# Performance work log

Measured on AMD Instinct MI355X. Metric: run time of the kernel, lower is better.

The kernel has to match this reference:

```python
import jax, jax.numpy as jnp
import numpy as np

B, S, D = 16, 1024, 384
H, DH = 6, 64  # head_dim = hidden // heads


def setup_inputs() -> dict:
    key = jax.random.key(0)
    ks = jax.random.split(key, 9)
    std = 0.02
    return {
        "x": jax.random.normal(ks[0], (B, S, D), jnp.float32),
        "Wq": jax.random.normal(ks[1], (H, D, DH), jnp.float32) * std,
        "bq": jax.random.normal(ks[2], (H, DH), jnp.float32) * std,
        "Wk": jax.random.normal(ks[3], (H, D, DH), jnp.float32) * std,
        "bk": jax.random.normal(ks[4], (H, DH), jnp.float32) * std,
        "Wv": jax.random.normal(ks[5], (H, D, DH), jnp.float32) * std,
        "bv": jax.random.normal(ks[6], (H, DH), jnp.float32) * std,
        "Wo": jax.random.normal(ks[7], (D, D), jnp.float32) * std,  # [out, in] like nn.Linear
        "bo": jax.random.normal(ks[8], (D,), jnp.float32) * std,
    }


def reference(x, Wq, bq, Wk, bk, Wv, bv, Wo, bo):
    # Per-head q/k/v projections (stacked over heads h)
    q = jnp.einsum("bsd,hde->bhse", x, Wq) + bq[None, :, None, :]
    k = jnp.einsum("bsd,hde->bhse", x, Wk) + bk[None, :, None, :]
    v = jnp.einsum("bsd,hde->bhse", x, Wv) + bv[None, :, None, :]
    # Explicit softmax attention (dropout prob = 0.0 in config)
    scores = jnp.einsum("bhse,bhte->bhst", q, k) / jnp.sqrt(jnp.float32(DH))
    probs = jax.nn.softmax(scores, axis=-1)
    ctx = jnp.einsum("bhst,bhte->bhse", probs, v)  # [B,H,S,DH]
    # Concat heads along last dim: [B,S,H*DH]
    concat = jnp.transpose(ctx, (0, 2, 1, 3)).reshape(B, S, H * DH)
    # Output projection (nn.Linear: y = x @ W^T + b)
    out = jnp.einsum("bsd,ed->bse", concat, Wo) + bo
    return out
```

## Files before the change

kernel.cpp:

```cpp
#include <hip/hip_runtime.h>
#include <hip/hip_bf16.h>

typedef __attribute__((ext_vector_type(8))) short short8;
typedef __attribute__((ext_vector_type(4))) short short4v;
typedef __attribute__((ext_vector_type(4))) float float4v;

#define MFMA16(a,b,c) __builtin_amdgcn_mfma_f32_16x16x32_bf16((a),(b),(c),0,0,0)
#define EXP2(x) __builtin_amdgcn_exp2f(x)

static constexpr int Bz = 16, Sq = 1024, Dm = 384, Hh = 6, Dh = 64;
static constexpr int Mtok = Bz * Sq;
static constexpr int NQKV = 1152;

__device__ __forceinline__ short f2bf(float f) {
  union { float f; unsigned u; } v; v.f = f;
  unsigned r = v.u + 0x7fffu + ((v.u >> 16) & 1u);
  return (short)(r >> 16);
}

__device__ __forceinline__ void gload16(const void* src, void* lds) {
  __builtin_amdgcn_global_load_lds(
      (const __attribute__((address_space(1))) unsigned int*)src,
      (__attribute__((address_space(3))) unsigned int*)lds, 16, 0, 0);
}

__global__ __launch_bounds__(256) void conv_x(const float* __restrict__ x,
                                              short* __restrict__ xb) {
  const int i = (blockIdx.x * 256 + threadIdx.x) * 8;
  float4v v0 = *(const float4v*)(x + i);
  float4v v1 = *(const float4v*)(x + i + 4);
  short8 o;
  o[0] = f2bf(v0[0]); o[1] = f2bf(v0[1]); o[2] = f2bf(v0[2]); o[3] = f2bf(v0[3]);
  o[4] = f2bf(v1[0]); o[5] = f2bf(v1[1]); o[6] = f2bf(v1[2]); o[7] = f2bf(v1[3]);
  *(short8*)(xb + i) = o;
}

__global__ __launch_bounds__(256) void conv_w(const float* __restrict__ Wq,
                                              const float* __restrict__ Wk,
                                              const float* __restrict__ Wv,
                                              const float* __restrict__ bq,
                                              const float* __restrict__ bk,
                                              const float* __restrict__ bv,
                                              const float* __restrict__ Wo,
                                              short* __restrict__ Wt,
                                              float* __restrict__ bias,
                                              short* __restrict__ Wob) {
  const float SCL = 0.125f * 1.44269504088896340736f;
  const int i = blockIdx.x * 256 + threadIdx.x;
  const int NW = NQKV * Dm;
  if (i < NW) {
    const int c = i / Dm, d = i % Dm;
    const int p = c / 384, rr = c % 384;
    const int h = rr >> 6, dh = rr & 63;
    const float* W = (p == 0) ? Wq : ((p == 1) ? Wk : Wv);
    float w = W[(h * Dm + d) * Dh + dh];
    if (p == 0) w *= SCL;
    Wt[c * Dm + d] = f2bf(w);
  } else if (i < NW + NQKV) {
    const int c = i - NW;
    const int p = c / 384, rr = c % 384;
    const int h = rr >> 6, dh = rr & 63;
    const float* bb = (p == 0) ? bq : ((p == 1) ? bk : bv);
    float b = bb[h * Dh + dh];
    if (p == 0) b *= SCL;
    bias[c] = b;
  } else if (i < NW + NQKV + Dm * Dm) {
    const int j = i - NW - NQKV;
    Wob[j] = f2bf(Wo[j]);
  }
}


__global__ __launch_bounds__(256) void qkv_gemm(const short* __restrict__ Xb,
                                                const short* __restrict__ Wt,
                                                const float* __restrict__ bias,
                                                short* __restrict__ qkv,
                                                short* __restrict__ vt) {
  __shared__ char smem[32768];
  const int tid = threadIdx.x;
  const int wave = tid >> 6, lane = tid & 63;
  const int r = lane & 15, g = lane >> 4;
  const int wr = wave >> 1, wc = wave & 1;

  const int flat = blockIdx.x;
  const int w = (flat & 7) * 144 + (flat >> 3);
  const int bx = w % 9, by = w / 9;
  const int bm0 = by * 128, bn0 = bx * 128;
  const int m0 = bm0 + wr * 64, n0 = bn0 + wc * 64;

  float bv_n[4];
#pragma unroll
  for (int ni = 0; ni < 4; ++ni) bv_n[ni] = bias[n0 + ni * 16 + r];
  asm volatile("s_waitcnt vmcnt(0)" ::: "memory");

  const char *aSrc0, *aSrc1, *bSrc0, *bSrc1;
  {
    const int o0 = tid * 16, o1 = 4096 + tid * 16;
    const int lr0 = o0 >> 7, cb0 = (o0 & 127) ^ ((lr0 & 7) << 4);
    const int lr1 = o1 >> 7, cb1 = (o1 & 127) ^ ((lr1 & 7) << 4);
    const int m_0 = 2 * lr0 + (cb0 >> 6), kb0 = cb0 & 63;
    const int m_1 = 2 * lr1 + (cb1 >> 6), kb1 = cb1 & 63;
    aSrc0 = (const char*)(Xb + (bm0 + m_0) * Dm) + kb0;
    aSrc1 = (const char*)(Xb + (bm0 + m_1) * Dm) + kb1;
    bSrc0 = (const char*)(Wt + (bn0 + m_0) * Dm) + kb0;
    bSrc1 = (const char*)(Wt + (bn0 + m_1) * Dm) + kb1;
  }
  auto stage = [&](int t, int buf) {
    char* base = smem + buf * 16384;
    const int kb = t * 64;
    gload16(aSrc0 + kb, base + wave * 1024);
    gload16(aSrc1 + kb, base + 4096 + wave * 1024);
    gload16(bSrc0 + kb, base + 8192 + wave * 1024);
    gload16(bSrc1 + kb, base + 12288 + wave * 1024);
  };

  int aOff[4], bOff[4];
#pragma unroll
  for (int i = 0; i < 4; ++i) {
    const int m = wr * 64 + i * 16 + r;
    const int lr = m >> 1;
    aOff[i] = lr * 128 + ((((m & 1) << 6) | (16 * g)) ^ ((lr & 7) << 4));
    const int n = wc * 64 + i * 16 + r;
    const int lrn = n >> 1;
    bOff[i] = 8192 + lrn * 128 + ((((n & 1) << 6) | (16 * g)) ^ ((lrn & 7) << 4));
  }

  float4v acc[4][4] = {};
  auto compute = [&](int buf) {
    const char* sb = smem + buf * 16384;
    short8 a[4], b[4];
#pragma unroll
    for (int i = 0; i < 4; ++i) a[i] = *(const short8*)(sb + aOff[i]);
#pragma unroll
    for (int i = 0; i < 4; ++i) b[i] = *(const short8*)(sb + bOff[i]);
#pragma unroll
    for (int mi = 0; mi < 4; ++mi)
#pragma unroll
      for (int ni = 0; ni < 4; ++ni)
        acc[mi][ni] = MFMA16(a[mi], b[ni], acc[mi][ni]);
  };

  stage(0, 0);
  stage(1, 1);
  for (int t = 0; t < 11; ++t) {
    asm volatile("s_waitcnt vmcnt(4)" ::: "memory");
    __builtin_amdgcn_s_barrier();
    compute(t & 1);
    __builtin_amdgcn_s_barrier();
    if (t < 10) stage(t + 2, t & 1);
  }
  asm volatile("s_waitcnt vmcnt(0)" ::: "memory");
  __builtin_amdgcn_s_barrier();
  compute(1);

#pragma unroll
  for (int ni = 0; ni < 4; ++ni) {
    const int col = n0 + ni * 16 + r;
    const int p = col / 384, rr2 = col % 384;
    const int h = rr2 >> 6, dh = rr2 & 63;
    const float bv = bv_n[ni];
#pragma unroll
    for (int mi = 0; mi < 4; ++mi) {
#pragma unroll
      for (int reg = 0; reg < 4; ++reg) {
        const int mg = m0 + mi * 16 + 4 * g + reg;
        const short o = f2bf(acc[mi][ni][reg] + bv);
        if (p < 2) {
          qkv[mg * NQKV + col] = o;
        } else {
          const int bb = mg >> 10, s = mg & 1023;
          vt[((bb * Hh + h) * Dh + dh) * Sq + s] = o;
        }
      }
    }
  }
}

__global__ __launch_bounds__(256) void attn(const short* __restrict__ qkv,
                                            const short* __restrict__ vt,
                                            short* __restrict__ ctx) {
  __shared__ char smem[32768];
  const int tid = threadIdx.x;
  const int wave = tid >> 6, lane = tid & 63;
  const int r = lane & 15, g = lane >> 4;
  const int xr = (r & 7) << 4;
  const int flat = blockIdx.x;
  const int w = (flat & 7) * 96 + (flat >> 3);
  const int qb = w & 7, bh = w >> 3;
  const int b = bh / Hh, h = bh % Hh;
  const int tok0 = b * Sq;
  const int qw = qb * 128 + wave * 32;

  short8 qf[2][2];
#pragma unroll
  for (int f = 0; f < 2; ++f) {
    const short* qp = qkv + (tok0 + qw + 16 * f + r) * NQKV + h * Dh;
    qf[f][0] = *(const short8*)(qp + 8 * g);
    qf[f][1] = *(const short8*)(qp + 32 + 8 * g);
  }
  asm volatile("s_waitcnt vmcnt(0)" ::: "memory");

  const short* kg = qkv + tok0 * NQKV + 384 + h * Dh;
  const short* vg = vt + (b * Hh + h) * Dh * Sq;

  const int o0 = wave * 2048 + lane * 16;
  const int row0 = o0 >> 7, cb0 = (o0 & 127) ^ ((row0 & 7) << 4);
  const int o1 = o0 + 1024;
  const int row1 = o1 >> 7, cb1 = (o1 & 127) ^ ((row1 & 7) << 4);

#define STAGE(T, BUFSEL)                                                        \
  {                                                                             \
    char* kb_ = smem + (BUFSEL) * 16384;                                        \
    const int kv_ = (T) * 64;                                                   \
    gload16((const char*)(kg + (kv_ + row0) * NQKV) + cb0, kb_ + wave * 2048);  \
    gload16((const char*)(vg + row0 * Sq + kv_) + cb0, kb_ + 8192 + wave * 2048);\
    gload16((const char*)(kg + (kv_ + row1) * NQKV) + cb1, kb_ + wave * 2048 + 1024);\
    gload16((const char*)(vg + row1 * Sq + kv_) + cb1, kb_ + 8192 + wave * 2048 + 1024);\
  }

  int kOff[4][2], vOff[4][2];
#pragma unroll
  for (int kt = 0; kt < 4; ++kt)
#pragma unroll
    for (int c = 0; c < 2; ++c)
      kOff[kt][c] = (16 * kt + r) * 128 + ((64 * c + 16 * g) ^ xr);
#pragma unroll
  for (int d = 0; d < 4; ++d)
#pragma unroll
    for (int h2 = 0; h2 < 2; ++h2)
      vOff[d][h2] = (16 * d + r) * 128 + ((64 * h2 + 8 * g) ^ xr);

  float4v acc[4][2] = {};
  float lsum[2] = {0.f, 0.f};

  auto compute = [&](int bufsel) {
    const char* kb = smem + bufsel * 16384;
    const char* vb = kb + 8192;
    short8 kf[4][2];
#pragma unroll
    for (int kt = 0; kt < 4; ++kt) {
      kf[kt][0] = *(const short8*)(kb + kOff[kt][0]);
      kf[kt][1] = *(const short8*)(kb + kOff[kt][1]);
    }
    short8 vf[4][2];
#pragma unroll
    for (int d = 0; d < 4; ++d)
#pragma unroll
      for (int h2 = 0; h2 < 2; ++h2) {
        short4v lo = *(const short4v*)(vb + vOff[d][h2]);
        short4v hi = *(const short4v*)(vb + (vOff[d][h2] ^ 32));
        short8 t;
        t[0] = lo[0]; t[1] = lo[1]; t[2] = lo[2]; t[3] = lo[3];
        t[4] = hi[0]; t[5] = hi[1]; t[6] = hi[2]; t[7] = hi[3];
        vf[d][h2] = t;
      }
    float4v s[4][2];
#pragma unroll
    for (int kt = 0; kt < 4; ++kt)
#pragma unroll
      for (int f = 0; f < 2; ++f) {
        float4v z = {};
        z = MFMA16(kf[kt][0], qf[f][0], z);
        z = MFMA16(kf[kt][1], qf[f][1], z);
        s[kt][f] = z;
      }
    short8 pa[2][2];
#pragma unroll
    for (int f = 0; f < 2; ++f) {
      float ps = 0.f;
#pragma unroll
      for (int h2 = 0; h2 < 2; ++h2) {
#pragma unroll
        for (int j = 0; j < 4; ++j) {
          const float e0 = EXP2(s[2 * h2][f][j]);
          const float e1 = EXP2(s[2 * h2 + 1][f][j]);
          pa[f][h2][j]     = f2bf(e0);
          pa[f][h2][4 + j] = f2bf(e1);
          ps += e0 + e1;
        }
      }
      lsum[f] += ps;
    }
#pragma unroll
    for (int d = 0; d < 4; ++d)
#pragma unroll
      for (int f = 0; f < 2; ++f) {
        acc[d][f] = MFMA16(pa[f][0], vf[d][0], acc[d][f]);
        acc[d][f] = MFMA16(pa[f][1], vf[d][1], acc[d][f]);
      }
  };

  STAGE(0, 0)
  STAGE(1, 1)
  for (int t = 0; t < 15; ++t) {
    asm volatile("s_waitcnt vmcnt(4)" ::: "memory");
    __builtin_amdgcn_s_barrier();
    compute(t & 1);
    __builtin_amdgcn_s_barrier();
    if (t < 14) STAGE(t + 2, t & 1)
  }
  asm volatile("s_waitcnt vmcnt(0)" ::: "memory");
  __builtin_amdgcn_s_barrier();
  compute(1);

#pragma unroll
  for (int f = 0; f < 2; ++f) {
    lsum[f] += __shfl_xor(lsum[f], 16);
    lsum[f] += __shfl_xor(lsum[f], 32);
  }
#pragma unroll
  for (int f = 0; f < 2; ++f) {
    float il[4];
#pragma unroll
    for (int reg = 0; reg < 4; ++reg) il[reg] = 1.f / __shfl(lsum[f], 4 * g + reg);
#pragma unroll
    for (int d = 0; d < 4; ++d) {
      short* cp = ctx + (tok0 + qw + 16 * f + 4 * g) * Dm + h * Dh + 16 * d + r;
#pragma unroll
      for (int reg = 0; reg < 4; ++reg)
        cp[reg * Dm] = f2bf(acc[d][f][reg] * il[reg]);
    }
  }
}

__global__ __launch_bounds__(256) void out_gemm(const short* __restrict__ ctx,
                                                const short* __restrict__ Wob,
                                                const float* __restrict__ bo,
                                                float* __restrict__ out) {
  __shared__ char smem[32768];
  const int tid = threadIdx.x;
  const int wave = tid >> 6, lane = tid & 63;
  const int r = lane & 15, g = lane >> 4;
  const int wr = wave >> 1, wc = wave & 1;

  const int flat = blockIdx.x;
  const int w = (flat & 7) * 48 + (flat >> 3);
  const int bx = w % 3, by = w / 3;
  const int bm0 = by * 128, bn0 = bx * 128;
  const int m0 = bm0 + wr * 64, n0 = bn0 + wc * 64;

  float bv_n[4];
#pragma unroll
  for (int ni = 0; ni < 4; ++ni) bv_n[ni] = bo[n0 + ni * 16 + r];
  asm volatile("s_waitcnt vmcnt(0)" ::: "memory");

  const char *aSrc0, *aSrc1, *bSrc0, *bSrc1;
  {
    const int o0 = tid * 16, o1 = 4096 + tid * 16;
    const int lr0 = o0 >> 7, cb0 = (o0 & 127) ^ ((lr0 & 7) << 4);
    const int lr1 = o1 >> 7, cb1 = (o1 & 127) ^ ((lr1 & 7) << 4);
    const int m_0 = 2 * lr0 + (cb0 >> 6), kb0 = cb0 & 63;
    const int m_1 = 2 * lr1 + (cb1 >> 6), kb1 = cb1 & 63;
    aSrc0 = (const char*)(ctx + (bm0 + m_0) * Dm) + kb0;
    aSrc1 = (const char*)(ctx + (bm0 + m_1) * Dm) + kb1;
    bSrc0 = (const char*)(Wob + (bn0 + m_0) * Dm) + kb0;
    bSrc1 = (const char*)(Wob + (bn0 + m_1) * Dm) + kb1;
  }
  auto stage = [&](int t, int buf) {
    char* base = smem + buf * 16384;
    const int kb = t * 64;
    gload16(aSrc0 + kb, base + wave * 1024);
    gload16(aSrc1 + kb, base + 4096 + wave * 1024);
    gload16(bSrc0 + kb, base + 8192 + wave * 1024);
    gload16(bSrc1 + kb, base + 12288 + wave * 1024);
  };

  int aOff[4], bOff[4];
#pragma unroll
  for (int i = 0; i < 4; ++i) {
    const int m = wr * 64 + i * 16 + r;
    const int lr = m >> 1;
    aOff[i] = lr * 128 + ((((m & 1) << 6) | (16 * g)) ^ ((lr & 7) << 4));
    const int n = wc * 64 + i * 16 + r;
    const int lrn = n >> 1;
    bOff[i] = 8192 + lrn * 128 + ((((n & 1) << 6) | (16 * g)) ^ ((lrn & 7) << 4));
  }

  float4v acc[4][4] = {};
  auto compute = [&](int buf) {
    const char* sb = smem + buf * 16384;
    short8 a[4], b[4];
#pragma unroll
    for (int i = 0; i < 4; ++i) a[i] = *(const short8*)(sb + aOff[i]);
#pragma unroll
    for (int i = 0; i < 4; ++i) b[i] = *(const short8*)(sb + bOff[i]);
#pragma unroll
    for (int mi = 0; mi < 4; ++mi)
#pragma unroll
      for (int ni = 0; ni < 4; ++ni)
        acc[mi][ni] = MFMA16(a[mi], b[ni], acc[mi][ni]);
  };

  stage(0, 0);
  stage(1, 1);
  for (int t = 0; t < 11; ++t) {
    asm volatile("s_waitcnt vmcnt(4)" ::: "memory");
    __builtin_amdgcn_s_barrier();
    compute(t & 1);
    __builtin_amdgcn_s_barrier();
    if (t < 10) stage(t + 2, t & 1);
  }
  asm volatile("s_waitcnt vmcnt(0)" ::: "memory");
  __builtin_amdgcn_s_barrier();
  compute(1);

#pragma unroll
  for (int ni = 0; ni < 4; ++ni) {
    const int col = n0 + ni * 16 + r;
    const float bv = bv_n[ni];
#pragma unroll
    for (int mi = 0; mi < 4; ++mi) {
#pragma unroll
      for (int reg = 0; reg < 4; ++reg) {
        const int mg = m0 + mi * 16 + 4 * g + reg;
        out[mg * Dm + col] = acc[mi][ni][reg] + bv;
      }
    }
  }
}

extern "C" void kernel_launch(void* const* d_in, const int* in_sizes, int n_in,
                              void* d_out, int out_size, void* d_ws, size_t ws_size,
                              hipStream_t stream) {
  const float* x  = (const float*)d_in[0];
  const float* Wq = (const float*)d_in[1];
  const float* bq = (const float*)d_in[2];
  const float* Wk = (const float*)d_in[3];
  const float* bk = (const float*)d_in[4];
  const float* Wv = (const float*)d_in[5];
  const float* bv = (const float*)d_in[6];
  const float* Wo = (const float*)d_in[7];
  const float* bo = (const float*)d_in[8];
  float* out = (float*)d_out;

  char* ws = (char*)d_ws;
  short* Xb   = (short*)(ws);
  short* Wt   = (short*)(ws + 12582912);
  float* bias = (float*)(ws + 13467648);
  short* Wob  = (short*)(ws + 13472256);
  short* qkv  = (short*)(ws + 13767168);
  short* vt   = (short*)(ws + 51515904);
  short* ctx  = (short*)(ws + 64098816);

  conv_x<<<Mtok * Dm / (256 * 8), 256, 0, stream>>>(x, Xb);
  conv_w<<<(NQKV * Dm + NQKV + Dm * Dm + 255) / 256, 256, 0, stream>>>(
      Wq, Wk, Wv, bq, bk, bv, Wo, Wt, bias, Wob);
  qkv_gemm<<<1152, 256, 0, stream>>>(Xb, Wt, bias, qkv, vt);
  attn<<<768, 256, 0, stream>>>(qkv, vt, ctx);
  out_gemm<<<384, 256, 0, stream>>>(ctx, Wob, bo, out);
}
```

Measured before the change: 114.2 us.

## Triple-buffer GEMM stages, use packed bf16 converts, and prioritize MFMA in attention

New measurement: 103.8 us. 1.1x faster.

```diff
diff --git a/kernel.cpp b/kernel.cpp
--- a/kernel.cpp
+++ b/kernel.cpp
@@ -4,6 +4,7 @@
 typedef __attribute__((ext_vector_type(8))) short short8;
 typedef __attribute__((ext_vector_type(4))) short short4v;
 typedef __attribute__((ext_vector_type(4))) float float4v;
+typedef __attribute__((ext_vector_type(4))) int int4v;
 
 #define MFMA16(a,b,c) __builtin_amdgcn_mfma_f32_16x16x32_bf16((a),(b),(c),0,0,0)
 #define EXP2(x) __builtin_amdgcn_exp2f(x)
@@ -16,6 +17,12 @@
   union { float f; unsigned u; } v; v.f = f;
   unsigned r = v.u + 0x7fffu + ((v.u >> 16) & 1u);
   return (short)(r >> 16);
+}
+
+__device__ __forceinline__ unsigned cvtpk(float a, float b) {
+  unsigned d;
+  asm("v_cvt_pk_bf16_f32 %0, %1, %2" : "=v"(d) : "v"(a), "v"(b));
+  return d;
 }
 
 __device__ __forceinline__ void gload16(const void* src, void* lds) {
@@ -76,7 +83,7 @@
                                                 const float* __restrict__ bias,
                                                 short* __restrict__ qkv,
                                                 short* __restrict__ vt) {
-  __shared__ char smem[32768];
+  __shared__ char smem[49152];
   const int tid = threadIdx.x;
   const int wave = tid >> 6, lane = tid & 63;
   const int r = lane & 15, g = lane >> 4;
@@ -142,16 +149,21 @@
 
   stage(0, 0);
   stage(1, 1);
-  for (int t = 0; t < 11; ++t) {
-    asm volatile("s_waitcnt vmcnt(4)" ::: "memory");
-    __builtin_amdgcn_s_barrier();
-    compute(t & 1);
-    __builtin_amdgcn_s_barrier();
-    if (t < 10) stage(t + 2, t & 1);
-  }
-  asm volatile("s_waitcnt vmcnt(0)" ::: "memory");
+  stage(2, 2);
+#pragma unroll 1
+  for (int t = 0; t < 10; ++t) {
+    asm volatile("s_waitcnt vmcnt(8)" ::: "memory");
+    __builtin_amdgcn_s_barrier();
+    compute(t % 3);
+    __builtin_amdgcn_s_barrier();
+    if (t < 9) stage(t + 3, t % 3);
+  }
+  asm volatile("s_waitcnt vmcnt(4)" ::: "memory");
   __builtin_amdgcn_s_barrier();
   compute(1);
+  asm volatile("s_waitcnt vmcnt(0)" ::: "memory");
+  __builtin_amdgcn_s_barrier();
+  compute(2);
 
 #pragma unroll
   for (int ni = 0; ni < 4; ++ni) {
@@ -162,14 +174,19 @@
 #pragma unroll
     for (int mi = 0; mi < 4; ++mi) {
 #pragma unroll
-      for (int reg = 0; reg < 4; ++reg) {
-        const int mg = m0 + mi * 16 + 4 * g + reg;
-        const short o = f2bf(acc[mi][ni][reg] + bv);
+      for (int rp = 0; rp < 2; ++rp) {
+        const unsigned u = cvtpk(acc[mi][ni][2 * rp] + bv,
+                                 acc[mi][ni][2 * rp + 1] + bv);
+        const short lo = (short)u, hi = (short)(u >> 16);
+        const int mg = m0 + mi * 16 + 4 * g + 2 * rp;
         if (p < 2) {
-          qkv[mg * NQKV + col] = o;
+          qkv[mg * NQKV + col] = lo;
+          qkv[(mg + 1) * NQKV + col] = hi;
         } else {
           const int bb = mg >> 10, s = mg & 1023;
-          vt[((bb * Hh + h) * Dh + dh) * Sq + s] = o;
+          short* vp = vt + ((bb * Hh + h) * Dh + dh) * Sq;
+          vp[s] = lo;
+          vp[s + 1] = hi;
         }
       }
     }
@@ -255,6 +272,7 @@
         vf[d][h2] = t;
       }
     float4v s[4][2];
+    __builtin_amdgcn_s_setprio(1);
 #pragma unroll
     for (int kt = 0; kt < 4; ++kt)
 #pragma unroll
@@ -264,23 +282,30 @@
         z = MFMA16(kf[kt][1], qf[f][1], z);
         s[kt][f] = z;
       }
+    __builtin_amdgcn_s_setprio(0);
     short8 pa[2][2];
 #pragma unroll
     for (int f = 0; f < 2; ++f) {
       float ps = 0.f;
 #pragma unroll
       for (int h2 = 0; h2 < 2; ++h2) {
+        float e0[4], e1[4];
 #pragma unroll
         for (int j = 0; j < 4; ++j) {
-          const float e0 = EXP2(s[2 * h2][f][j]);
-          const float e1 = EXP2(s[2 * h2 + 1][f][j]);
-          pa[f][h2][j]     = f2bf(e0);
-          pa[f][h2][4 + j] = f2bf(e1);
-          ps += e0 + e1;
+          e0[j] = EXP2(s[2 * h2][f][j]);
+          e1[j] = EXP2(s[2 * h2 + 1][f][j]);
+          ps += e0[j] + e1[j];
         }
+        int4v wv;
+        wv[0] = (int)cvtpk(e0[0], e0[1]);
+        wv[1] = (int)cvtpk(e0[2], e0[3]);
+        wv[2] = (int)cvtpk(e1[0], e1[1]);
+        wv[3] = (int)cvtpk(e1[2], e1[3]);
+        pa[f][h2] = __builtin_bit_cast(short8, wv);
       }
       lsum[f] += ps;
     }
+    __builtin_amdgcn_s_setprio(1);
 #pragma unroll
     for (int d = 0; d < 4; ++d)
 #pragma unroll
@@ -288,10 +313,12 @@
         acc[d][f] = MFMA16(pa[f][0], vf[d][0], acc[d][f]);
         acc[d][f] = MFMA16(pa[f][1], vf[d][1], acc[d][f]);
       }
+    __builtin_amdgcn_s_setprio(0);
   };
 
   STAGE(0, 0)
   STAGE(1, 1)
+#pragma unroll 1
   for (int t = 0; t < 15; ++t) {
     asm volatile("s_waitcnt vmcnt(4)" ::: "memory");
     __builtin_amdgcn_s_barrier();
@@ -327,7 +354,7 @@
                                                 const short* __restrict__ Wob,
                                                 const float* __restrict__ bo,
                                                 float* __restrict__ out) {
-  __shared__ char smem[32768];
+  __shared__ char smem[49152];
   const int tid = threadIdx.x;
   const int wave = tid >> 6, lane = tid & 63;
   const int r = lane & 15, g = lane >> 4;
@@ -393,16 +420,21 @@
 
   stage(0, 0);
   stage(1, 1);
-  for (int t = 0; t < 11; ++t) {
-    asm volatile("s_waitcnt vmcnt(4)" ::: "memory");
-    __builtin_amdgcn_s_barrier();
-    compute(t & 1);
-    __builtin_amdgcn_s_barrier();
-    if (t < 10) stage(t + 2, t & 1);
-  }
-  asm volatile("s_waitcnt vmcnt(0)" ::: "memory");
+  stage(2, 2);
+#pragma unroll 1
+  for (int t = 0; t < 10; ++t) {
+    asm volatile("s_waitcnt vmcnt(8)" ::: "memory");
+    __builtin_amdgcn_s_barrier();
+    compute(t % 3);
+    __builtin_amdgcn_s_barrier();
+    if (t < 9) stage(t + 3, t % 3);
+  }
+  asm volatile("s_waitcnt vmcnt(4)" ::: "memory");
   __builtin_amdgcn_s_barrier();
   compute(1);
+  asm volatile("s_waitcnt vmcnt(0)" ::: "memory");
+  __builtin_amdgcn_s_barrier();
+  compute(2);
 
 #pragma unroll
   for (int ni = 0; ni < 4; ++ni) {
```
